# Performance work log

Hardware: AMD Instinct MI355X
Metric: run time of the kernel (lower is better)

## Reference

```python
import jax, jax.numpy as jnp
import numpy as np

SIDE_LEN = 128
RESOLUTION = 1.0  # Angstrom per pixel


def setup_inputs() -> dict:
    key = jax.random.key(0)
    k1, k2, k3 = jax.random.split(key, 3)
    B, A = 16, 20000
    # atom xyz coords in Angstrom, spread within the field of view (+/- 63.5 A)
    mol = jax.random.normal(k1, (B, A, 3), dtype=jnp.float32) * 20.0
    # per-atom Gaussian std in [0.5, 1.5) A (strictly positive)
    stds = jax.random.uniform(k2, (A,), dtype=jnp.float32) + 0.5
    # per-atom density (mass) in [0.5, 1.5)
    densities = jax.random.uniform(k3, (A,), dtype=jnp.float32) + 0.5
    return {"mol": mol, "stds": stds, "densities": densities}


def reference(mol, stds, densities):
    # Pixel-center coordinate grid, identical to torch.arange(-x_max, x_max+1e-5, res)
    x_max = (SIDE_LEN - 1) * RESOLUTION / 2
    coord = jnp.arange(-x_max, x_max + 1e-5, RESOLUTION, dtype=jnp.float32)  # (S,)
    var = stds * stds                              # (A,)
    neg_half_inv_var = (-0.5 / var)[None, :, None] # (1,A,1)
    # Separable Gaussian profiles: exp(-(coord - mu)^2 / (2 var))
    dx = coord[None, None, :] - mol[:, :, 0:1]     # (B,A,S) x-offsets
    dy = coord[None, None, :] - mol[:, :, 1:2]     # (B,A,S) y-offsets
    gx = jnp.exp(neg_half_inv_var * dx * dx)       # (B,A,W)
    gy = jnp.exp(neg_half_inv_var * dy * dy)       # (B,A,H)
    coef = densities / (2.0 * jnp.pi * var)        # (A,)
    # img[b,h,w] = sum_a coef_a * gy[b,a,h] * gx[b,a,w]  (batched matmul)
    img = jnp.einsum('bah,baw->bhw', gy * coef[None, :, None], gx)
    return img  # (B, SIDE_LEN, SIDE_LEN)
```

## Files before the change

kernel.cpp:

```cpp
#include <hip/hip_runtime.h>


#define S 128
#define NS 32
#define PER 640
#define BLOCK 512

typedef _Float16 f16;
typedef _Float16 f16x2 __attribute__((ext_vector_type(2)));
typedef _Float16 f16x8 __attribute__((ext_vector_type(8)));
typedef float floatx16 __attribute__((ext_vector_type(16)));

#if __has_builtin(__builtin_amdgcn_exp2f)
#define FAST_EXP2(x) __builtin_amdgcn_exp2f(x)
#else
#define FAST_EXP2(x) exp2f(x)
#endif
#if __has_builtin(__builtin_amdgcn_rcpf)
#define FAST_RCP(x) __builtin_amdgcn_rcpf(x)
#else
#define FAST_RCP(x) (1.0f / (x))
#endif

static __device__ __forceinline__ f16x2 PKRTZ(float a, float b) {
#if __has_builtin(__builtin_amdgcn_cvt_pkrtz)
    return __builtin_bit_cast(f16x2, __builtin_amdgcn_cvt_pkrtz(a, b));
#else
    return (f16x2){(f16)a, (f16)b};
#endif
}

union frag_u { f16x8 v; f16x2 h[4]; };

__global__ __launch_bounds__(BLOCK, 4) void k_proj(
    const float* __restrict__ mol,
    const float* __restrict__ stds,
    const float* __restrict__ dens,
    f16* __restrict__ part,
    int B, int A)
{
    __shared__ float4 sP[PER];
    __shared__ float red[4 * 4096];

    const int ks   = blockIdx.x;
    const int b    = blockIdx.y;
    const int tid  = threadIdx.x;
    const int lane = tid & 63;
    const int wav  = tid >> 6;
    const int quad = wav & 3;
    const int half = wav >> 2;
    const int l31  = lane & 31;
    const int hi   = lane >> 5;

    const int a0  = ks * PER;
    const int a1  = min(a0 + PER, A);
    const int cnt = a1 - a0;

    for (int i = tid; i < cnt; i += BLOCK) {
        const int a = a0 + i;
        const size_t idx = (size_t)b * A + a;
        float x  = mol[idx * 3 + 0];
        float y  = mol[idx * 3 + 1];
        float v  = stds[a] * stds[a];
        float rv = FAST_RCP(v);
        sP[i] = make_float4(x, y, -0.72134752044448f * rv,
                            __log2f(dens[a] * 0.15915494309189535f * rv));
    }
    __syncthreads();

    const int hcnt = cnt >> 1;
    const int nk   = hcnt >> 4;

    const float py0 = (float)((quad >> 1) * 64 + l31) - 63.5f;
    const float px0 = (float)((quad & 1) * 64 + l31) - 63.5f;

    floatx16 acc[2][2];
#pragma unroll
    for (int rr = 0; rr < 2; ++rr)
#pragma unroll
        for (int cb = 0; cb < 2; ++cb) acc[rr][cb] = (floatx16){0.f};

    const float4* sp = sP + half * hcnt + hi * 8;

    for (int s = 0; s < nk; ++s) {
        const float4* pp = sp + (size_t)s * 16;
        frag_u A0, A1, B0, B1;
#pragma unroll
        for (int jp = 0; jp < 4; ++jp) {
            float ea0[2], ea1[2], eb0[2], eb1[2];
#pragma unroll
            for (int u = 0; u < 2; ++u) {
                float4 p = pp[2 * jp + u];
                float dy = py0 - p.y;
                float t  = p.z * dy;
                float g0 = fmaf(t, dy, p.w);
                float g1 = fmaf(1024.0f, p.z, fmaf(64.0f, t, g0));
                ea0[u] = FAST_EXP2(g0);
                ea1[u] = FAST_EXP2(g1);
                float dx = px0 - p.x;
                float sx = p.z * dx;
                float h0 = sx * dx;
                float h1 = fmaf(1024.0f, p.z, fmaf(64.0f, sx, h0));
                eb0[u] = FAST_EXP2(h0);
                eb1[u] = FAST_EXP2(h1);
            }
            A0.h[jp] = PKRTZ(ea0[0], ea0[1]);
            A1.h[jp] = PKRTZ(ea1[0], ea1[1]);
            B0.h[jp] = PKRTZ(eb0[0], eb0[1]);
            B1.h[jp] = PKRTZ(eb1[0], eb1[1]);
        }
        acc[0][0] = __builtin_amdgcn_mfma_f32_32x32x16_f16(A0.v, B0.v, acc[0][0], 0, 0, 0);
        acc[0][1] = __builtin_amdgcn_mfma_f32_32x32x16_f16(A0.v, B1.v, acc[0][1], 0, 0, 0);
        acc[1][0] = __builtin_amdgcn_mfma_f32_32x32x16_f16(A1.v, B0.v, acc[1][0], 0, 0, 0);
        acc[1][1] = __builtin_amdgcn_mfma_f32_32x32x16_f16(A1.v, B1.v, acc[1][1], 0, 0, 0);
    }

    float* rq = red + quad * 4096;
    if (half == 0) {
#pragma unroll
        for (int rr = 0; rr < 2; ++rr)
#pragma unroll
            for (int cb = 0; cb < 2; ++cb) {
                float* t = rq + (rr * 2 + cb) * 1024 + lane;
#pragma unroll
                for (int j = 0; j < 16; ++j) t[j * 64] = acc[rr][cb][j];
            }
    }
    __syncthreads();

    if (half == 1) {
        f16* base = part + ((size_t)(b * NS + ks)) * (S * S) + lane * 16;
#pragma unroll
        for (int rr = 0; rr < 2; ++rr)
#pragma unroll
            for (int cb = 0; cb < 2; ++cb) {
                float* t = rq + (rr * 2 + cb) * 1024 + lane;
                floatx16 v = acc[rr][cb];
#pragma unroll
                for (int j = 0; j < 16; ++j) v[j] += t[j * 64];
                const int tileidx = ((quad >> 1) * 2 + rr) * 4 + ((quad & 1) * 2 + cb);
                f16* pq = base + (size_t)tileidx * 1024;
                frag_u lo, hiv;
#pragma unroll
                for (int jp = 0; jp < 4; ++jp) {
                    lo.h[jp]  = PKRTZ(v[2 * jp],     v[2 * jp + 1]);
                    hiv.h[jp] = PKRTZ(v[2 * jp + 8], v[2 * jp + 9]);
                }
                *(f16x8*)(pq + 0) = lo.v;
                *(f16x8*)(pq + 8) = hiv.v;
            }
    }
}

__global__ __launch_bounds__(256) void k_reduce(const f16* __restrict__ part,
                                                float* __restrict__ out) {
    const int b  = blockIdx.z;
    const int f8 = (blockIdx.x * 256 + threadIdx.x) * 8;

    const f16* src = part + (size_t)b * NS * (S * S) + f8;
    float s0[8] = {0.f}, s1[8] = {0.f};
    for (int s = 0; s < NS; s += 2) {
        f16x8 v0 = *(const f16x8*)&src[(size_t)s * (S * S)];
        f16x8 v1 = *(const f16x8*)&src[(size_t)(s + 1) * (S * S)];
#pragma unroll
        for (int i = 0; i < 8; ++i) { s0[i] += (float)v0[i]; s1[i] += (float)v1[i]; }
    }

    const int reg0 = f8 & 15;
    const int lane = (f8 >> 4) & 63;
    const int tile = f8 >> 10;
    const int r    = tile >> 2;
    const int cc   = tile & 3;
    const int rowb = r * 32 + 4 * (lane >> 5);
    const int col  = cc * 32 + (lane & 31);
#pragma unroll
    for (int i = 0; i < 8; ++i) {
        const int reg = reg0 + i;
        const int row = rowb + (reg & 3) + 8 * (reg >> 2);
        out[((size_t)b * S + row) * S + col] = s0[i] + s1[i];
    }
}

extern "C" void kernel_launch(void* const* d_in, const int* in_sizes, int n_in,
                              void* d_out, int out_size, void* d_ws, size_t ws_size,
                              hipStream_t stream) {
    const float* mol  = (const float*)d_in[0];
    const float* stds = (const float*)d_in[1];
    const float* dens = (const float*)d_in[2];
    float* out = (float*)d_out;

    const int A = in_sizes[1];
    const int B = in_sizes[0] / (A * 3);

    f16* part = (f16*)d_ws;

    k_proj<<<dim3(NS, B), dim3(BLOCK), 0, stream>>>(mol, stds, dens, part, B, A);
    k_reduce<<<dim3((S * S) / (256 * 8), 1, B), dim3(256), 0, stream>>>(part, out);
}
```

Baseline: 93.49 us.

## Generate Gaussian profiles once per chunk into shared memory and reuse across waves

Previously each wave computed its own exp values for its 64-row and 64-column slices, so the same Gaussian profiles were recomputed by several waves. Now the waves cooperatively generate the per-axis profiles for 32-atom chunks into double-buffered LDS tiles, and the MFMA loop reads its fragments from LDS. This reduces redundant exp work at the cost of LDS traffic and a barrier per chunk. The reduce kernel is also reworked so that four waves each sum a quarter of the split partials and combine them through LDS, giving more blocks and more parallel loads.

Result: faster. 87.98 us (-5.9%).

```diff
diff --git a/kernel.cpp b/kernel.cpp
--- a/kernel.cpp
+++ b/kernel.cpp
@@ -5,6 +5,8 @@
 #define NS 32
 #define PER 640
 #define BLOCK 512
+#define KC 32
+#define GSTR 40
 
 typedef _Float16 f16;
 typedef _Float16 f16x2 __attribute__((ext_vector_type(2)));
@@ -32,6 +34,14 @@
 
 union frag_u { f16x8 v; f16x2 h[4]; };
 
+union SharedU {
+    struct {
+        float4 sG[2][PER];
+        f16 g[2][2][S * GSTR];
+    } m;
+    float red[4 * 4096];
+};
+
 __global__ __launch_bounds__(BLOCK, 4) void k_proj(
     const float* __restrict__ mol,
     const float* __restrict__ stds,
@@ -39,8 +49,7 @@
     f16* __restrict__ part,
     int B, int A)
 {
-    __shared__ float4 sP[PER];
-    __shared__ float red[4 * 4096];
+    __shared__ SharedU sh;
 
     const int ks   = blockIdx.x;
     const int b    = blockIdx.y;
@@ -63,16 +72,22 @@
         float y  = mol[idx * 3 + 1];
         float v  = stds[a] * stds[a];
         float rv = FAST_RCP(v);
-        sP[i] = make_float4(x, y, -0.72134752044448f * rv,
-                            __log2f(dens[a] * 0.15915494309189535f * rv));
-    }
-    __syncthreads();
-
-    const int hcnt = cnt >> 1;
-    const int nk   = hcnt >> 4;
-
-    const float py0 = (float)((quad >> 1) * 64 + l31) - 63.5f;
-    const float px0 = (float)((quad & 1) * 64 + l31) - 63.5f;
+        float z  = -0.72134752044448f * rv;
+        float w  = __log2f(dens[a] * 0.15915494309189535f * rv);
+        sh.m.sG[0][i] = make_float4(x, z, 0.f, 0.f);
+        sh.m.sG[1][i] = make_float4(y, z, w,   0.f);
+    }
+    __syncthreads();
+
+    const int nc = cnt >> 5;
+
+    const int gaxis = wav >> 2;
+    const int agrp  = wav & 3;
+    const float c0  = (float)lane - 63.5f;
+
+    const int arow = (quad >> 1) * 64 + l31;
+    const int acol = (quad & 1) * 64 + l31;
+    const int aoff = half * 16 + hi * 8;
 
     floatx16 acc[2][2];
 #pragma unroll
@@ -80,42 +95,51 @@
 #pragma unroll
         for (int cb = 0; cb < 2; ++cb) acc[rr][cb] = (floatx16){0.f};
 
-    const float4* sp = sP + half * hcnt + hi * 8;
-
-    for (int s = 0; s < nk; ++s) {
-        const float4* pp = sp + (size_t)s * 16;
+    auto GEN = [&](int c, int buf) {
+        const float4* prm = &sh.m.sG[gaxis][c * KC + agrp * 8];
+        f16* dst = &sh.m.g[buf][gaxis][lane * GSTR + agrp * 8];
+        frag_u V0, V1;
+#pragma unroll
+        for (int i2 = 0; i2 < 4; ++i2) {
+            float e0[2], e1[2];
+#pragma unroll
+            for (int u = 0; u < 2; ++u) {
+                float4 p = prm[i2 * 2 + u];
+                float d  = c0 - p.x;
+                float t  = p.y * d;
+                float g0 = fmaf(t, d, p.z);
+                float g1 = fmaf(128.0f, t, fmaf(4096.0f, p.y, g0));
+                e0[u] = FAST_EXP2(g0);
+                e1[u] = FAST_EXP2(g1);
+            }
+            V0.h[i2] = PKRTZ(e0[0], e0[1]);
+            V1.h[i2] = PKRTZ(e1[0], e1[1]);
+        }
+        *(f16x8*)dst                = V0.v;
+        *(f16x8*)(dst + 64 * GSTR)  = V1.v;
+    };
+
+    GEN(0, 0);
+    __syncthreads();
+
+    for (int c = 0; c < nc; ++c) {
+        const int cb = c & 1;
+        const f16* gy = sh.m.g[cb][1];
+        const f16* gx = sh.m.g[cb][0];
         frag_u A0, A1, B0, B1;
-#pragma unroll
-        for (int jp = 0; jp < 4; ++jp) {
-            float ea0[2], ea1[2], eb0[2], eb1[2];
-#pragma unroll
-            for (int u = 0; u < 2; ++u) {
-                float4 p = pp[2 * jp + u];
-                float dy = py0 - p.y;
-                float t  = p.z * dy;
-                float g0 = fmaf(t, dy, p.w);
-                float g1 = fmaf(1024.0f, p.z, fmaf(64.0f, t, g0));
-                ea0[u] = FAST_EXP2(g0);
-                ea1[u] = FAST_EXP2(g1);
-                float dx = px0 - p.x;
-                float sx = p.z * dx;
-                float h0 = sx * dx;
-                float h1 = fmaf(1024.0f, p.z, fmaf(64.0f, sx, h0));
-                eb0[u] = FAST_EXP2(h0);
-                eb1[u] = FAST_EXP2(h1);
-            }
-            A0.h[jp] = PKRTZ(ea0[0], ea0[1]);
-            A1.h[jp] = PKRTZ(ea1[0], ea1[1]);
-            B0.h[jp] = PKRTZ(eb0[0], eb0[1]);
-            B1.h[jp] = PKRTZ(eb1[0], eb1[1]);
-        }
+        A0.v = *(const f16x8*)(gy + arow * GSTR + aoff);
+        A1.v = *(const f16x8*)(gy + (arow + 32) * GSTR + aoff);
+        B0.v = *(const f16x8*)(gx + acol * GSTR + aoff);
+        B1.v = *(const f16x8*)(gx + (acol + 32) * GSTR + aoff);
         acc[0][0] = __builtin_amdgcn_mfma_f32_32x32x16_f16(A0.v, B0.v, acc[0][0], 0, 0, 0);
         acc[0][1] = __builtin_amdgcn_mfma_f32_32x32x16_f16(A0.v, B1.v, acc[0][1], 0, 0, 0);
         acc[1][0] = __builtin_amdgcn_mfma_f32_32x32x16_f16(A1.v, B0.v, acc[1][0], 0, 0, 0);
         acc[1][1] = __builtin_amdgcn_mfma_f32_32x32x16_f16(A1.v, B1.v, acc[1][1], 0, 0, 0);
-    }
-
-    float* rq = red + quad * 4096;
+        if (c + 1 < nc) GEN(c + 1, cb ^ 1);
+        __syncthreads();
+    }
+
+    float* rq = sh.red + quad * 4096;
     if (half == 0) {
 #pragma unroll
         for (int rr = 0; rr < 2; ++rr)
@@ -154,30 +178,46 @@
 
 __global__ __launch_bounds__(256) void k_reduce(const f16* __restrict__ part,
                                                 float* __restrict__ out) {
-    const int b  = blockIdx.z;
-    const int f8 = (blockIdx.x * 256 + threadIdx.x) * 8;
-
-    const f16* src = part + (size_t)b * NS * (S * S) + f8;
-    float s0[8] = {0.f}, s1[8] = {0.f};
-    for (int s = 0; s < NS; s += 2) {
-        f16x8 v0 = *(const f16x8*)&src[(size_t)s * (S * S)];
-        f16x8 v1 = *(const f16x8*)&src[(size_t)(s + 1) * (S * S)];
-#pragma unroll
-        for (int i = 0; i < 8; ++i) { s0[i] += (float)v0[i]; s1[i] += (float)v1[i]; }
-    }
-
-    const int reg0 = f8 & 15;
-    const int lane = (f8 >> 4) & 63;
-    const int tile = f8 >> 10;
-    const int r    = tile >> 2;
-    const int cc   = tile & 3;
-    const int rowb = r * 32 + 4 * (lane >> 5);
-    const int col  = cc * 32 + (lane & 31);
-#pragma unroll
-    for (int i = 0; i < 8; ++i) {
-        const int reg = reg0 + i;
-        const int row = rowb + (reg & 3) + 8 * (reg >> 2);
-        out[((size_t)b * S + row) * S + col] = s0[i] + s1[i];
+    __shared__ float lred[3][64][9];
+    const int b    = blockIdx.z;
+    const int lane = threadIdx.x & 63;
+    const int w    = threadIdx.x >> 6;
+    const int f8   = (blockIdx.x * 64 + lane) * 8;
+
+    const f16* src = part + (size_t)b * NS * (S * S) + (size_t)(w * 8) * (S * S) + f8;
+    float s[8] = {0.f};
+#pragma unroll
+    for (int t = 0; t < 8; ++t) {
+        f16x8 v = *(const f16x8*)&src[(size_t)t * (S * S)];
+#pragma unroll
+        for (int i = 0; i < 8; ++i) s[i] += (float)v[i];
+    }
+
+    if (w) {
+#pragma unroll
+        for (int i = 0; i < 8; ++i) lred[w - 1][lane][i] = s[i];
+    }
+    __syncthreads();
+
+    if (w == 0) {
+#pragma unroll
+        for (int j = 0; j < 3; ++j)
+#pragma unroll
+            for (int i = 0; i < 8; ++i) s[i] += lred[j][lane][i];
+
+        const int reg0   = f8 & 15;
+        const int lane_f = (f8 >> 4) & 63;
+        const int tile   = f8 >> 10;
+        const int r      = tile >> 2;
+        const int cc     = tile & 3;
+        const int rowb = r * 32 + 4 * (lane_f >> 5);
+        const int col  = cc * 32 + (lane_f & 31);
+#pragma unroll
+        for (int i = 0; i < 8; ++i) {
+            const int reg = reg0 + i;
+            const int row = rowb + (reg & 3) + 8 * (reg >> 2);
+            out[((size_t)b * S + row) * S + col] = s[i];
+        }
     }
 }
 
@@ -195,5 +235,5 @@
     f16* part = (f16*)d_ws;
 
     k_proj<<<dim3(NS, B), dim3(BLOCK), 0, stream>>>(mol, stds, dens, part, B, A);
-    k_reduce<<<dim3((S * S) / (256 * 8), 1, B), dim3(256), 0, stream>>>(part, out);
-}
+    k_reduce<<<dim3((S * S) / (64 * 8), 1, B), dim3(256), 0, stream>>>(part, out);
+}
```
